# Kernel tuning notes

Measured on AMD Instinct MI355X. Metric: run time of the kernel, lower is better.

The kernel has to match this reference:

```python
import jax, jax.numpy as jnp
import numpy as np


def _layernorm(x, g, b, eps=1e-5):
    mu = jnp.mean(x, axis=-1, keepdims=True)
    xc = x - mu
    var = jnp.mean(xc * xc, axis=-1, keepdims=True)
    return xc * jax.lax.rsqrt(var + eps) * g + b


def _s5(u, Lambda_re, Lambda_im, B_re, B_im, C_re, C_im, Dskip, log_step):
    # Diagonal complex SSM with ZOH discretization (S5).
    Lam = Lambda_re + 1j * Lambda_im                       # (P,) complex64
    Lam_bar = jnp.exp(Lam * jnp.exp(log_step))             # (P,)
    B_bar = ((Lam_bar - 1.0) / Lam)[:, None] * (B_re + 1j * B_im)  # (P, D)
    Bu = jnp.einsum('bld,pd->blp', u.astype(jnp.complex64), B_bar)  # (B, L, P)
    A = jnp.broadcast_to(Lam_bar, Bu.shape)

    def combine(e1, e2):
        a1, b1 = e1
        a2, b2 = e2
        return a1 * a2, a2 * b1 + b2

    _, xs = jax.lax.associative_scan(combine, (A, Bu), axis=1)  # parallel scan over L
    y = 2.0 * jnp.real(jnp.einsum('blp,dp->bld', xs, C_re + 1j * C_im))
    return y + Dskip * u


def setup_inputs() -> dict:
    key = jax.random.key(0)
    ks = jax.random.split(key, 10)
    B, L, D, P = 4, 2048, 1024, 64
    F = int(D * 2.0)  # ff_mult = 2.0
    x = jax.random.normal(ks[0], (B, L, D), jnp.float32)
    ln1_g = jnp.ones((D,), jnp.float32)
    ln1_b = jnp.zeros((D,), jnp.float32)
    ln2_g = jnp.ones((D,), jnp.float32)
    ln2_b = jnp.zeros((D,), jnp.float32)
    Lambda_re = -(0.5 + jax.random.uniform(ks[1], (P,), jnp.float32))  # stable poles
    Lambda_im = jnp.pi * jnp.arange(P, dtype=jnp.float32)              # HiPPO-like spread
    B_re = jax.random.normal(ks[2], (P, D), jnp.float32) / np.float32(np.sqrt(D))
    B_im = jax.random.normal(ks[3], (P, D), jnp.float32) / np.float32(np.sqrt(D))
    C_re = jax.random.normal(ks[4], (D, P), jnp.float32) / np.float32(np.sqrt(P))
    C_im = jax.random.normal(ks[5], (D, P), jnp.float32) / np.float32(np.sqrt(P))
    Dskip = jax.random.normal(ks[6], (D,), jnp.float32)
    dt_min, dt_max = 1e-3, 1e-1
    log_step = (np.float32(np.log(dt_min))
                + jax.random.uniform(ks[7], (P,), jnp.float32)
                * np.float32(np.log(dt_max) - np.log(dt_min)))
    W_enc = jax.random.normal(ks[8], (2 * F, D), jnp.float32) / np.float32(np.sqrt(D))
    W_dec = jax.random.normal(ks[9], (D, F), jnp.float32) / np.float32(np.sqrt(F))
    return dict(x=x, ln1_g=ln1_g, ln1_b=ln1_b, ln2_g=ln2_g, ln2_b=ln2_b,
                Lambda_re=Lambda_re, Lambda_im=Lambda_im, B_re=B_re, B_im=B_im,
                C_re=C_re, C_im=C_im, Dskip=Dskip, log_step=log_step,
                W_enc=W_enc, W_dec=W_dec)


def reference(x, ln1_g, ln1_b, ln2_g, ln2_b, Lambda_re, Lambda_im, B_re, B_im,
              C_re, C_im, Dskip, log_step, W_enc, W_dec):
    # S5Block: pre-LN -> S5 -> GELU -> residual (dropout = identity in eval)
    fx = _layernorm(x, ln1_g, ln1_b)
    h = jax.nn.gelu(_s5(fx, Lambda_re, Lambda_im, B_re, B_im, C_re, C_im, Dskip, log_step),
                    approximate=False) + fx
    # pre-LN GEGLU feed-forward -> residual
    fx2 = _layernorm(h, ln2_g, ln2_b)
    e = fx2 @ W_enc.T                      # (B, L, 2F)
    a, gate = jnp.split(e, 2, axis=-1)
    e = a * jax.nn.gelu(gate, approximate=False)
    return e @ W_dec.T + fx2
```

## Files before the change

### kernel.cpp

```cpp
#include <hip/hip_runtime.h>
#include <hip/hip_bf16.h>
#include <math.h>

typedef unsigned short u16;
typedef __bf16 v8bf __attribute__((ext_vector_type(8)));
typedef float f32x4 __attribute__((ext_vector_type(4)));

__device__ __forceinline__ float us2f(u16 h) {
    union { unsigned int u; float f; } v; v.u = ((unsigned int)h) << 16; return v.f;
}
__device__ __forceinline__ u16 f2us(float f) {
    union { float f; unsigned int u; } v; v.f = f;
    unsigned int r = v.u + 0x7fffu + ((v.u >> 16) & 1u);
    return (u16)(r >> 16);
}
__device__ __forceinline__ float gelu_f(float x) {
    return 0.5f * x * (1.0f + erff(x * 0.70710678118654752f));
}
__device__ __forceinline__ void gload_lds16(const u16* g, u16* l) {
    auto gp = reinterpret_cast<const __attribute__((address_space(1))) unsigned int*>(
        (uintptr_t)g);
    auto lp = reinterpret_cast<__attribute__((address_space(3))) unsigned int*>(
        (uintptr_t)l);
    __builtin_amdgcn_global_load_lds(gp, lp, 16, 0, 0);
}

__global__ __launch_bounds__(256) void cvt_kernel(const float* __restrict__ in,
                                                  u16* __restrict__ out, int n)
{
    const int i = (blockIdx.x * 256 + threadIdx.x) * 8;
    if (i >= n) return;
    float4 a = *reinterpret_cast<const float4*>(in + i);
    float4 b = *reinterpret_cast<const float4*>(in + i + 4);
    u16 o[8] = { f2us(a.x), f2us(a.y), f2us(a.z), f2us(a.w),
                 f2us(b.x), f2us(b.y), f2us(b.z), f2us(b.w) };
    *reinterpret_cast<uint4*>(out + i) = *reinterpret_cast<uint4*>(o);
}

template<typename TIN>
__global__ __launch_bounds__(256) void ln_kernel(const TIN* __restrict__ in,
                                                 const float* __restrict__ g,
                                                 const float* __restrict__ b,
                                                 u16* __restrict__ out)
{
    const int row = blockIdx.x, tid = threadIdx.x;
    const size_t base = (size_t)row * 1024 + tid * 4;
    float x0, x1, x2, x3;
    if constexpr (sizeof(TIN) == 4) {
        float4 v = *reinterpret_cast<const float4*>(in + base);
        x0 = v.x; x1 = v.y; x2 = v.z; x3 = v.w;
    } else {
        ushort4 v = *reinterpret_cast<const ushort4*>((const u16*)in + base);
        x0 = us2f(v.x); x1 = us2f(v.y); x2 = us2f(v.z); x3 = us2f(v.w);
    }
    float s = x0 + x1 + x2 + x3;
    float q = x0*x0 + x1*x1 + x2*x2 + x3*x3;
    #pragma unroll
    for (int o = 32; o; o >>= 1) { s += __shfl_down(s, o); q += __shfl_down(q, o); }
    __shared__ float red[8];
    if ((tid & 63) == 0) { red[tid >> 6] = s; red[4 + (tid >> 6)] = q; }
    __syncthreads();
    s = red[0] + red[1] + red[2] + red[3];
    q = red[4] + red[5] + red[6] + red[7];
    const float mu = s * (1.0f / 1024.0f);
    const float rs = rsqrtf(q * (1.0f / 1024.0f) - mu * mu + 1e-5f);
    float4 gv = *reinterpret_cast<const float4*>(g + tid * 4);
    float4 bv = *reinterpret_cast<const float4*>(b + tid * 4);
    ushort4 o4;
    o4.x = f2us((x0 - mu) * rs * gv.x + bv.x);
    o4.y = f2us((x1 - mu) * rs * gv.y + bv.y);
    o4.z = f2us((x2 - mu) * rs * gv.z + bv.z);
    o4.w = f2us((x3 - mu) * rs * gv.w + bv.w);
    *reinterpret_cast<ushort4*>(out + base) = o4;
}

__global__ __launch_bounds__(256) void prep_kernel(
    const float* __restrict__ Lre, const float* __restrict__ Lim, const float* __restrict__ lstep,
    const float* __restrict__ Bre, const float* __restrict__ Bim,
    const float* __restrict__ Cre, const float* __restrict__ Cim,
    u16* __restrict__ Bbar, u16* __restrict__ C2)
{
    const int idx = blockIdx.x * 256 + threadIdx.x;
    if (idx < 65536) {
        const int p = idx >> 10, d = idx & 1023;
        const float lr = Lre[p], li = Lim[p];
        const float dt = expf(lstep[p]);
        const float er = expf(lr * dt);
        const float ar = er * cosf(li * dt), ai = er * sinf(li * dt);
        const float nr = ar - 1.0f, ni = ai;
        const float den = lr * lr + li * li;
        const float cr = (nr * lr + ni * li) / den;
        const float ci = (ni * lr - nr * li) / den;
        const float br = Bre[idx], bi = Bim[idx];
        Bbar[p * 1024 + d]        = f2us(cr * br - ci * bi);
        Bbar[(64 + p) * 1024 + d] = f2us(cr * bi + ci * br);
    } else {
        const int i = idx - 65536;
        const int d = i >> 6, p = i & 63;
        C2[d * 128 + p]      = f2us( 2.0f * Cre[i]);
        C2[d * 128 + 64 + p] = f2us(-2.0f * Cim[i]);
    }
}

__global__ __launch_bounds__(256) void scan_kernel(
    const float* __restrict__ Bu,
    const float* __restrict__ Lre, const float* __restrict__ Lim, const float* __restrict__ lstep,
    u16* __restrict__ A2)
{
    const int b = blockIdx.x >> 6;
    const int p = blockIdx.x & 63;
    const int t = threadIdx.x;
    const float lr = Lre[p], li = Lim[p];
    const float dt = expf(lstep[p]);
    const float er = expf(lr * dt);
    const float ar = er * cosf(li * dt), ai = er * sinf(li * dt);

    const size_t base = ((size_t)b * 2048 + t * 8) * 128;
    float xr[8], xi[8];
    float sr = 0.f, si = 0.f;
    #pragma unroll
    for (int i = 0; i < 8; ++i) {
        const float br = Bu[base + i * 128 + p];
        const float bi = Bu[base + i * 128 + 64 + p];
        const float nr = ar * sr - ai * si + br;
        const float ni = ar * si + ai * sr + bi;
        sr = nr; si = ni;
        xr[i] = sr; xi[i] = si;
    }
    float fr = ar, fi = ai;
    #pragma unroll
    for (int s = 0; s < 3; ++s) { const float t2 = fr*fr - fi*fi; fi = 2.f*fr*fi; fr = t2; }
    __shared__ float Er[256], Ei[256];
    Er[t] = sr; Ei[t] = si;
    __syncthreads();
    float vr = sr, vi = si;
    for (int off = 1; off < 256; off <<= 1) {
        float pr = 0.f, pi = 0.f;
        if (t >= off) { pr = Er[t - off]; pi = Ei[t - off]; }
        __syncthreads();
        vr += fr * pr - fi * pi;
        vi += fr * pi + fi * pr;
        Er[t] = vr; Ei[t] = vi;
        const float nf = fr*fr - fi*fi; fi = 2.f*fr*fi; fr = nf;
        __syncthreads();
    }
    float cr = 0.f, ci = 0.f;
    if (t > 0) { cr = Er[t - 1]; ci = Ei[t - 1]; }
    float gr = ar * cr - ai * ci, gi = ar * ci + ai * cr;
    #pragma unroll
    for (int i = 0; i < 8; ++i) {
        xr[i] += gr; xi[i] += gi;
        const float n2 = ar * gr - ai * gi; gi = ar * gi + ai * gr; gr = n2;
    }
    #pragma unroll
    for (int i = 0; i < 8; ++i) {
        const size_t m = (size_t)b * 2048 + t * 8 + i;
        A2[m * 128 + p]      = f2us(xr[i]);
        A2[m * 128 + 64 + p] = f2us(xi[i]);
    }
}

template<int BM, int BN>
__global__ __launch_bounds__(64) void gemm_small_kernel(
    const u16* __restrict__ A, const u16* __restrict__ B, float* __restrict__ Cout,
    const int N, const int K)
{
    __shared__ u16 lsA[BM * 32];
    __shared__ u16 lsB[BN * 32];
    const int tid = threadIdx.x;
    const int lane = tid & 63;
    const int m0 = blockIdx.y * BM, n0 = blockIdx.x * BN;
    f32x4 acc[4][4] = {};
    for (int k0 = 0; k0 < K; k0 += 32) {
        #pragma unroll
        for (int j = 0; j < 4; ++j) {
            const int s = j * 64 + tid;
            gload_lds16(A + (size_t)(m0 + (s >> 2)) * K + k0 + (s & 3) * 8,
                        lsA + (s - lane) * 8);
            gload_lds16(B + (size_t)(n0 + (s >> 2)) * K + k0 + (s & 3) * 8,
                        lsB + (s - lane) * 8);
        }
        __syncthreads();
        v8bf af[4], bfv[4];
        #pragma unroll
        for (int f = 0; f < 4; ++f)
            af[f] = *reinterpret_cast<const v8bf*>(
                lsA + (f * 16 + (lane & 15)) * 32 + (lane >> 4) * 8);
        #pragma unroll
        for (int f = 0; f < 4; ++f)
            bfv[f] = *reinterpret_cast<const v8bf*>(
                lsB + (f * 16 + (lane & 15)) * 32 + (lane >> 4) * 8);
        #pragma unroll
        for (int fm = 0; fm < 4; ++fm)
            #pragma unroll
            for (int fn = 0; fn < 4; ++fn)
                acc[fm][fn] = __builtin_amdgcn_mfma_f32_16x16x32_bf16(
                    af[fm], bfv[fn], acc[fm][fn], 0, 0, 0);
        __syncthreads();
    }
    #pragma unroll
    for (int fm = 0; fm < 4; ++fm)
    #pragma unroll
    for (int fn = 0; fn < 4; ++fn)
    #pragma unroll
    for (int i = 0; i < 4; ++i) {
        const int r = m0 + fm * 16 + (lane >> 4) * 4 + i;
        const int c = n0 + fn * 16 + (lane & 15);
        Cout[(size_t)r * N + c] = acc[fm][fn][i];
    }
}

template<bool GLU>
__device__ __forceinline__ void stage_half(u16* ldsbuf,
    const u16* __restrict__ A, const u16* __restrict__ Bm,
    int half, int tile, int m0, int n0, int K, int NO, int wid, int lane)
{
    const int k0 = tile * 64;
    #pragma unroll
    for (int j = 0; j < 2; ++j) {
        const int chunk = wid * 2 + j;
        const int rloc  = chunk * 8 + (lane >> 3);
        const int sslot = (lane & 7) ^ ((lane >> 3) & 7);
        const u16* src;
        int ldsrow0;
        if (half < 2) {
            ldsrow0 = half * 128 + chunk * 8;
            src = A + (size_t)(m0 + half * 128 + rloc) * K + k0 + sslot * 8;
        } else {
            const int rb = (half - 2) * 128 + rloc;
            ldsrow0 = 256 + (half - 2) * 128 + chunk * 8;
            const int grow = GLU ? ((half == 2) ? (n0 + rb) : (NO + n0 + rb - 128))
                                 : (n0 + rb);
            src = Bm + (size_t)grow * K + k0 + sslot * 8;
        }
        gload_lds16(src, ldsbuf + ldsrow0 * 64);
    }
}

template<int BROWS, int EPI, int NBX>
__global__ __launch_bounds__(512, 2) void gemm8p_kernel(
    const u16* __restrict__ A, const u16* __restrict__ Bm, void* __restrict__ Cout,
    const int K, const int NO, const int NT,
    const u16* __restrict__ aux, const float* __restrict__ dskip)
{
    constexpr bool GLU = (EPI == 2);
    __shared__ u16 lds[2][(256 + BROWS) * 64];

    const int tid  = threadIdx.x;
    const int lane = tid & 63;
    const int wid  = tid >> 6;
    const int wm   = wid >> 2;
    const int wn   = wid & 3;
    const int l15 = lane & 15, lg = lane >> 4, l7 = lane & 7;

    const int bid = blockIdx.x;
    const int swz = (bid & 7) * (NBX * 4) + (bid >> 3);
    const int by = swz / NBX, bx = swz % NBX;
    const int m0 = by * 256, n0 = bx * 128;

    f32x4 accA[8][2] = {};
    f32x4 accG[8][2] = {};

    constexpr int S_HALF[8] = {0, 1, 2, 3, 0, 1, 2, 3};
    constexpr int S_OFS [8] = {1, 1, 2, 2, 2, 2, 3, 3};

    #pragma unroll
    for (int t = 0; t < 2; ++t)
        #pragma unroll
        for (int h = 0; h < (GLU ? 4 : 3); ++h)
            stage_half<GLU>((u16*)lds[t], A, Bm, h, t, m0, n0, K, NO, wid, lane);
    asm volatile("s_waitcnt vmcnt(0)" ::: "memory");
    __builtin_amdgcn_s_barrier();

    const int NI = NT >> 1;
    for (int i = 0; i < NI; ++i) {
        #pragma unroll
        for (int hb = 0; hb < 2; ++hb) {
            const u16* cb = (const u16*)lds[hb];
            v8bf bf[2][2][2];
            #pragma unroll
            for (int p = 0; p < 4; ++p) {
                v8bf af[2][2];
                #pragma unroll
                for (int j = 0; j < 2; ++j) {
                    const int row = wm * 128 + (p * 2 + j) * 16 + l15;
                    #pragma unroll
                    for (int kk = 0; kk < 2; ++kk) {
                        const int phys = (kk * 4 + lg) ^ l7;
                        af[j][kk] = *reinterpret_cast<const v8bf*>(
                            cb + row * 64 + phys * 8);
                    }
                }
                if (p == 0) {
                    #pragma unroll
                    for (int cf = 0; cf < 2; ++cf)
                    #pragma unroll
                    for (int ag = 0; ag < (GLU ? 2 : 1); ++ag)
                    #pragma unroll
                    for (int kk = 0; kk < 2; ++kk) {
                        const int rb = ag * 128 + wn * 32 + cf * 16 + l15;
                        const int phys = (kk * 4 + lg) ^ l7;
                        bf[cf][ag][kk] = *reinterpret_cast<const v8bf*>(
                            cb + (256 + rb) * 64 + phys * 8);
                    }
                }
                {
                    const int ph = hb * 4 + p;
                    const int ofs = S_OFS[ph], sh = S_HALF[ph];
                    const int tgt = 2 * i + ofs;
                    bool dost = (ofs == 1) ? (i > 0) : (tgt < NT);
                    if (!GLU && sh == 3) dost = false;
                    if (dost)
                        stage_half<GLU>((u16*)lds[tgt & 1], A, Bm, sh, tgt,
                                        m0, n0, K, NO, wid, lane);
                }
                __builtin_amdgcn_s_barrier();
                asm volatile("s_waitcnt lgkmcnt(0)" ::: "memory");
                __builtin_amdgcn_sched_barrier(0);
                __builtin_amdgcn_s_setprio(1);
                #pragma unroll
                for (int j = 0; j < 2; ++j) {
                    const int mf = p * 2 + j;
                    #pragma unroll
                    for (int cf = 0; cf < 2; ++cf)
                    #pragma unroll
                    for (int kk = 0; kk < 2; ++kk) {
                        accA[mf][cf] = __builtin_amdgcn_mfma_f32_16x16x32_bf16(
                            af[j][kk], bf[cf][0][kk], accA[mf][cf], 0, 0, 0);
                        if constexpr (GLU)
                            accG[mf][cf] = __builtin_amdgcn_mfma_f32_16x16x32_bf16(
                                af[j][kk], bf[cf][1][kk], accG[mf][cf], 0, 0, 0);
                    }
                }
                __builtin_amdgcn_s_setprio(0);
                if (p == 3) {
                    const int keept = 2 * i + 2 + hb;
                    if (keept < NT) {
                        if constexpr (GLU)
                            asm volatile("s_waitcnt vmcnt(4)" ::: "memory");
                        else
                            asm volatile("s_waitcnt vmcnt(2)" ::: "memory");
                    } else {
                        asm volatile("s_waitcnt vmcnt(0)" ::: "memory");
                    }
                }
                __builtin_amdgcn_s_barrier();
            }
        }
    }

    #pragma unroll
    for (int mf = 0; mf < 8; ++mf)
    #pragma unroll
    for (int cf = 0; cf < 2; ++cf)
    #pragma unroll
    for (int q = 0; q < 4; ++q) {
        const int r = m0 + wm * 128 + mf * 16 + lg * 4 + q;
        const int c = n0 + wn * 32 + cf * 16 + l15;
        const size_t o = (size_t)r * NO + c;
        const float v = accA[mf][cf][q];
        if constexpr (EPI == 2) {
            ((u16*)Cout)[o] = f2us(v * gelu_f(accG[mf][cf][q]));
        } else if constexpr (EPI == 1) {
            const float u = us2f(aux[o]);
            const float t2 = v + dskip[c] * u;
            ((u16*)Cout)[o] = f2us(gelu_f(t2) + u);
        } else {
            ((float*)Cout)[o] = v + us2f(aux[o]);
        }
    }
}

static constexpr size_t OFF_FX  = 0;
static constexpr size_t OFF_BU  = 16777216;
static constexpr size_t OFF_A2  = 20971520;
static constexpr size_t OFF_E2  = 0;
static constexpr size_t OFF_FX2 = 33554432;
static constexpr size_t OFF_BB  = 50331648;
static constexpr size_t OFF_C2  = 50593792;
static constexpr size_t OFF_WE  = 50855936;
static constexpr size_t OFF_WD  = 59244544;

extern "C" void kernel_launch(void* const* d_in, const int* in_sizes, int n_in,
                              void* d_out, int out_size, void* d_ws, size_t ws_size,
                              hipStream_t stream) {
    const float* x    = (const float*)d_in[0];
    const float* l1g  = (const float*)d_in[1];
    const float* l1b  = (const float*)d_in[2];
    const float* l2g  = (const float*)d_in[3];
    const float* l2b  = (const float*)d_in[4];
    const float* Lre  = (const float*)d_in[5];
    const float* Lim  = (const float*)d_in[6];
    const float* Bre  = (const float*)d_in[7];
    const float* Bim  = (const float*)d_in[8];
    const float* Cre  = (const float*)d_in[9];
    const float* Cim  = (const float*)d_in[10];
    const float* Dsk  = (const float*)d_in[11];
    const float* lst  = (const float*)d_in[12];
    const float* Wenc = (const float*)d_in[13];
    const float* Wdec = (const float*)d_in[14];
    float* out = (float*)d_out;

    char* ws = (char*)d_ws;
    u16*   fx   = (u16*)(ws + OFF_FX);
    float* Bu   = (float*)(ws + OFF_BU);
    u16*   A2   = (u16*)(ws + OFF_A2);
    u16*   e2   = (u16*)(ws + OFF_E2);
    u16*   fx2  = (u16*)(ws + OFF_FX2);
    u16*   Bbar = (u16*)(ws + OFF_BB);
    u16*   C2   = (u16*)(ws + OFF_C2);
    u16*   WeB  = (u16*)(ws + OFF_WE);
    u16*   WdB  = (u16*)(ws + OFF_WD);
    u16*   h    = (u16*)d_out;

    ln_kernel<float><<<8192, 256, 0, stream>>>(x, l1g, l1b, fx);
    cvt_kernel<<<2048, 256, 0, stream>>>(Wenc, WeB, 4096 * 1024);
    cvt_kernel<<<1024, 256, 0, stream>>>(Wdec, WdB, 1024 * 2048);
    prep_kernel<<<512, 256, 0, stream>>>(Lre, Lim, lst, Bre, Bim, Cre, Cim, Bbar, C2);
    gemm_small_kernel<64, 64><<<dim3(2, 128), 64, 0, stream>>>(
        fx, Bbar, Bu, 128, 1024);
    scan_kernel<<<256, 256, 0, stream>>>(Bu, Lre, Lim, lst, A2);
    gemm8p_kernel<128, 1, 8><<<256, 512, 0, stream>>>(
        A2, C2, h, 128, 1024, 2, fx, Dsk);
    ln_kernel<u16><<<8192, 256, 0, stream>>>(h, l2g, l2b, fx2);
    gemm8p_kernel<256, 2, 16><<<512, 512, 0, stream>>>(
        fx2, WeB, e2, 1024, 2048, 16, nullptr, nullptr);
    gemm8p_kernel<128, 3, 8><<<256, 512, 0, stream>>>(
        e2, WdB, out, 2048, 1024, 32, fx2, nullptr);

    (void)in_sizes; (void)n_in; (void)out_size; (void)ws_size;
}
```

Before: 220.8 us.

## Specialize GEMM kernels into GEGLU 8-phase and plain 4-phase pipelines, merge prep kernels

Splits the generic templated GEMM into two kernels. One is a GEGLU-specific kernel with an unrolled 8-phase schedule and precomputed, incrementing staging pointers. The other is a plain GEMM kernel with a 4-phase schedule that reads 4 A fragments per phase and uses a smaller LDS buffer. It also fuses the two weight-conversion launches and the SSM parameter prep into a single kernel to cut launch overhead. The intent is to reduce address arithmetic and barrier count in the hot loops. The coarser phases may expose more latency or raise register pressure.

```diff
diff --git a/kernel.cpp b/kernel.cpp
--- a/kernel.cpp
+++ b/kernel.cpp
@@ -25,62 +25,28 @@
     __builtin_amdgcn_global_load_lds(gp, lp, 16, 0, 0);
 }
 
-__global__ __launch_bounds__(256) void cvt_kernel(const float* __restrict__ in,
-                                                  u16* __restrict__ out, int n)
-{
-    const int i = (blockIdx.x * 256 + threadIdx.x) * 8;
-    if (i >= n) return;
-    float4 a = *reinterpret_cast<const float4*>(in + i);
-    float4 b = *reinterpret_cast<const float4*>(in + i + 4);
-    u16 o[8] = { f2us(a.x), f2us(a.y), f2us(a.z), f2us(a.w),
-                 f2us(b.x), f2us(b.y), f2us(b.z), f2us(b.w) };
-    *reinterpret_cast<uint4*>(out + i) = *reinterpret_cast<uint4*>(o);
-}
-
-template<typename TIN>
-__global__ __launch_bounds__(256) void ln_kernel(const TIN* __restrict__ in,
-                                                 const float* __restrict__ g,
-                                                 const float* __restrict__ b,
-                                                 u16* __restrict__ out)
-{
-    const int row = blockIdx.x, tid = threadIdx.x;
-    const size_t base = (size_t)row * 1024 + tid * 4;
-    float x0, x1, x2, x3;
-    if constexpr (sizeof(TIN) == 4) {
-        float4 v = *reinterpret_cast<const float4*>(in + base);
-        x0 = v.x; x1 = v.y; x2 = v.z; x3 = v.w;
-    } else {
-        ushort4 v = *reinterpret_cast<const ushort4*>((const u16*)in + base);
-        x0 = us2f(v.x); x1 = us2f(v.y); x2 = us2f(v.z); x3 = us2f(v.w);
-    }
-    float s = x0 + x1 + x2 + x3;
-    float q = x0*x0 + x1*x1 + x2*x2 + x3*x3;
-    #pragma unroll
-    for (int o = 32; o; o >>= 1) { s += __shfl_down(s, o); q += __shfl_down(q, o); }
-    __shared__ float red[8];
-    if ((tid & 63) == 0) { red[tid >> 6] = s; red[4 + (tid >> 6)] = q; }
-    __syncthreads();
-    s = red[0] + red[1] + red[2] + red[3];
-    q = red[4] + red[5] + red[6] + red[7];
-    const float mu = s * (1.0f / 1024.0f);
-    const float rs = rsqrtf(q * (1.0f / 1024.0f) - mu * mu + 1e-5f);
-    float4 gv = *reinterpret_cast<const float4*>(g + tid * 4);
-    float4 bv = *reinterpret_cast<const float4*>(b + tid * 4);
-    ushort4 o4;
-    o4.x = f2us((x0 - mu) * rs * gv.x + bv.x);
-    o4.y = f2us((x1 - mu) * rs * gv.y + bv.y);
-    o4.z = f2us((x2 - mu) * rs * gv.z + bv.z);
-    o4.w = f2us((x3 - mu) * rs * gv.w + bv.w);
-    *reinterpret_cast<ushort4*>(out + base) = o4;
-}
-
-__global__ __launch_bounds__(256) void prep_kernel(
-    const float* __restrict__ Lre, const float* __restrict__ Lim, const float* __restrict__ lstep,
+__global__ __launch_bounds__(256) void prepall_kernel(
+    const float* __restrict__ Wenc, u16* __restrict__ WeB,
+    const float* __restrict__ Wdec, u16* __restrict__ WdB,
+    const float* __restrict__ Lre, const float* __restrict__ Lim,
+    const float* __restrict__ lstep,
     const float* __restrict__ Bre, const float* __restrict__ Bim,
     const float* __restrict__ Cre, const float* __restrict__ Cim,
     u16* __restrict__ Bbar, u16* __restrict__ C2)
 {
-    const int idx = blockIdx.x * 256 + threadIdx.x;
+    const int b = blockIdx.x, tid = threadIdx.x;
+    if (b < 3072) {
+        const float* in = (b < 2048) ? Wenc : Wdec;
+        u16* outp = (b < 2048) ? WeB : WdB;
+        const int i = (b < 2048 ? b : b - 2048) * 2048 + tid * 8;
+        float4 a = *reinterpret_cast<const float4*>(in + i);
+        float4 c = *reinterpret_cast<const float4*>(in + i + 4);
+        u16 o[8] = { f2us(a.x), f2us(a.y), f2us(a.z), f2us(a.w),
+                     f2us(c.x), f2us(c.y), f2us(c.z), f2us(c.w) };
+        *reinterpret_cast<uint4*>(outp + i) = *reinterpret_cast<uint4*>(o);
+        return;
+    }
+    const int idx = (b - 3072) * 256 + tid;
     if (idx < 65536) {
         const int p = idx >> 10, d = idx & 1023;
         const float lr = Lre[p], li = Lim[p];
@@ -102,9 +68,47 @@
     }
 }
 
+template<typename TIN>
+__global__ __launch_bounds__(256) void ln_kernel(const TIN* __restrict__ in,
+                                                 const float* __restrict__ g,
+                                                 const float* __restrict__ b,
+                                                 u16* __restrict__ out)
+{
+    const int row = blockIdx.x, tid = threadIdx.x;
+    const size_t base = (size_t)row * 1024 + tid * 4;
+    float x0, x1, x2, x3;
+    if constexpr (sizeof(TIN) == 4) {
+        float4 v = *reinterpret_cast<const float4*>(in + base);
+        x0 = v.x; x1 = v.y; x2 = v.z; x3 = v.w;
+    } else {
+        ushort4 v = *reinterpret_cast<const ushort4*>((const u16*)in + base);
+        x0 = us2f(v.x); x1 = us2f(v.y); x2 = us2f(v.z); x3 = us2f(v.w);
+    }
+    float s = x0 + x1 + x2 + x3;
+    float q = x0*x0 + x1*x1 + x2*x2 + x3*x3;
+    #pragma unroll
+    for (int o = 32; o; o >>= 1) { s += __shfl_down(s, o); q += __shfl_down(q, o); }
+    __shared__ float red[8];
+    if ((tid & 63) == 0) { red[tid >> 6] = s; red[4 + (tid >> 6)] = q; }
+    __syncthreads();
+    s = red[0] + red[1] + red[2] + red[3];
+    q = red[4] + red[5] + red[6] + red[7];
+    const float mu = s * (1.0f / 1024.0f);
+    const float rs = rsqrtf(q * (1.0f / 1024.0f) - mu * mu + 1e-5f);
+    float4 gv = *reinterpret_cast<const float4*>(g + tid * 4);
+    float4 bv = *reinterpret_cast<const float4*>(b + tid * 4);
+    ushort4 o4;
+    o4.x = f2us((x0 - mu) * rs * gv.x + bv.x);
+    o4.y = f2us((x1 - mu) * rs * gv.y + bv.y);
+    o4.z = f2us((x2 - mu) * rs * gv.z + bv.z);
+    o4.w = f2us((x3 - mu) * rs * gv.w + bv.w);
+    *reinterpret_cast<ushort4*>(out + base) = o4;
+}
+
 __global__ __launch_bounds__(256) void scan_kernel(
     const float* __restrict__ Bu,
-    const float* __restrict__ Lre, const float* __restrict__ Lim, const float* __restrict__ lstep,
+    const float* __restrict__ Lre, const float* __restrict__ Lim,
+    const float* __restrict__ lstep,
     u16* __restrict__ A2)
 {
     const int b = blockIdx.x >> 6;
@@ -210,143 +214,254 @@
     }
 }
 
-template<bool GLU>
-__device__ __forceinline__ void stage_half(u16* ldsbuf,
-    const u16* __restrict__ A, const u16* __restrict__ Bm,
-    int half, int tile, int m0, int n0, int K, int NO, int wid, int lane)
-{
-    const int k0 = tile * 64;
+#define BAR_MMA_BEGIN \
+    __builtin_amdgcn_s_barrier(); \
+    asm volatile("s_waitcnt lgkmcnt(0)" ::: "memory"); \
+    __builtin_amdgcn_sched_barrier(0); \
+    __builtin_amdgcn_s_setprio(1);
+#define MMA_END  __builtin_amdgcn_s_setprio(0);
+#define ENDBAR   __builtin_amdgcn_s_barrier();
+#define VMK(n)   asm volatile("s_waitcnt vmcnt(" #n ")" ::: "memory");
+
+#define STAGE(s, bi) do { \
+    u16* d0_ = lds + (bi) * BUFE + ((s) * 128 + (wid * 2 + 0) * 8) * 64; \
+    u16* d1_ = lds + (bi) * BUFE + ((s) * 128 + (wid * 2 + 1) * 8) * 64; \
+    gload_lds16(pS[s][0], d0_); gload_lds16(pS[s][1], d1_); \
+    pS[s][0] += 64; pS[s][1] += 64; } while (0)
+
+template<int MFB>
+__device__ __forceinline__ void glu_read_a(const u16* cb, int wm, int l15, int lg,
+                                           int l7, v8bf (&af)[2][2])
+{
     #pragma unroll
     for (int j = 0; j < 2; ++j) {
-        const int chunk = wid * 2 + j;
-        const int rloc  = chunk * 8 + (lane >> 3);
-        const int sslot = (lane & 7) ^ ((lane >> 3) & 7);
-        const u16* src;
-        int ldsrow0;
-        if (half < 2) {
-            ldsrow0 = half * 128 + chunk * 8;
-            src = A + (size_t)(m0 + half * 128 + rloc) * K + k0 + sslot * 8;
-        } else {
-            const int rb = (half - 2) * 128 + rloc;
-            ldsrow0 = 256 + (half - 2) * 128 + chunk * 8;
-            const int grow = GLU ? ((half == 2) ? (n0 + rb) : (NO + n0 + rb - 128))
-                                 : (n0 + rb);
-            src = Bm + (size_t)grow * K + k0 + sslot * 8;
-        }
-        gload_lds16(src, ldsbuf + ldsrow0 * 64);
-    }
-}
-
-template<int BROWS, int EPI, int NBX>
-__global__ __launch_bounds__(512, 2) void gemm8p_kernel(
-    const u16* __restrict__ A, const u16* __restrict__ Bm, void* __restrict__ Cout,
-    const int K, const int NO, const int NT,
-    const u16* __restrict__ aux, const float* __restrict__ dskip)
-{
-    constexpr bool GLU = (EPI == 2);
-    __shared__ u16 lds[2][(256 + BROWS) * 64];
-
-    const int tid  = threadIdx.x;
-    const int lane = tid & 63;
-    const int wid  = tid >> 6;
-    const int wm   = wid >> 2;
-    const int wn   = wid & 3;
+        const int row = wm * 128 + (MFB + j) * 16 + l15;
+        #pragma unroll
+        for (int kk = 0; kk < 2; ++kk)
+            af[j][kk] = *reinterpret_cast<const v8bf*>(
+                cb + row * 64 + (((kk * 4 + lg) ^ l7) * 8));
+    }
+}
+__device__ __forceinline__ void glu_read_b(const u16* cb, int wn, int l15, int lg,
+                                           int l7, v8bf (&bf)[2][2][2])
+{
+    #pragma unroll
+    for (int cf = 0; cf < 2; ++cf)
+    #pragma unroll
+    for (int ag = 0; ag < 2; ++ag)
+    #pragma unroll
+    for (int kk = 0; kk < 2; ++kk) {
+        const int rb = ag * 128 + wn * 32 + cf * 16 + l15;
+        bf[cf][ag][kk] = *reinterpret_cast<const v8bf*>(
+            cb + (256 + rb) * 64 + (((kk * 4 + lg) ^ l7) * 8));
+    }
+}
+template<int MFB>
+__device__ __forceinline__ void glu_mma(const v8bf (&af)[2][2], const v8bf (&bf)[2][2][2],
+                                        f32x4 (&accA)[8][2], f32x4 (&accG)[8][2])
+{
+    #pragma unroll
+    for (int j = 0; j < 2; ++j)
+    #pragma unroll
+    for (int cf = 0; cf < 2; ++cf)
+    #pragma unroll
+    for (int kk = 0; kk < 2; ++kk) {
+        accA[MFB + j][cf] = __builtin_amdgcn_mfma_f32_16x16x32_bf16(
+            af[j][kk], bf[cf][0][kk], accA[MFB + j][cf], 0, 0, 0);
+        accG[MFB + j][cf] = __builtin_amdgcn_mfma_f32_16x16x32_bf16(
+            af[j][kk], bf[cf][1][kk], accG[MFB + j][cf], 0, 0, 0);
+    }
+}
+
+template<int NBX>
+__global__ __launch_bounds__(512, 2) void geglu8p_kernel(
+    const u16* __restrict__ A, const u16* __restrict__ Bm, u16* __restrict__ Cout,
+    const int K, const int NO, const int NT)
+{
+    constexpr int BUFE = 512 * 64;
+    __shared__ u16 lds[2 * BUFE];
+    const int tid = threadIdx.x, lane = tid & 63, wid = tid >> 6;
+    const int wm = wid >> 2, wn = wid & 3;
     const int l15 = lane & 15, lg = lane >> 4, l7 = lane & 7;
-
     const int bid = blockIdx.x;
     const int swz = (bid & 7) * (NBX * 4) + (bid >> 3);
     const int by = swz / NBX, bx = swz % NBX;
     const int m0 = by * 256, n0 = bx * 128;
 
+    const int rl = lane >> 3;
+    const int scol = ((lane & 7) ^ rl) * 8;
+    const u16* pS[4][2];
+    #pragma unroll
+    for (int j = 0; j < 2; ++j) {
+        const int rloc = (wid * 2 + j) * 8 + rl;
+        pS[0][j] = A  + (size_t)(m0 + rloc)       * K + scol;
+        pS[1][j] = A  + (size_t)(m0 + 128 + rloc) * K + scol;
+        pS[2][j] = Bm + (size_t)(n0 + rloc)       * K + scol;
+        pS[3][j] = Bm + (size_t)(NO + n0 + rloc)  * K + scol;
+    }
+
     f32x4 accA[8][2] = {};
     f32x4 accG[8][2] = {};
 
-    constexpr int S_HALF[8] = {0, 1, 2, 3, 0, 1, 2, 3};
-    constexpr int S_OFS [8] = {1, 1, 2, 2, 2, 2, 3, 3};
-
-    #pragma unroll
-    for (int t = 0; t < 2; ++t)
-        #pragma unroll
-        for (int h = 0; h < (GLU ? 4 : 3); ++h)
-            stage_half<GLU>((u16*)lds[t], A, Bm, h, t, m0, n0, K, NO, wid, lane);
-    asm volatile("s_waitcnt vmcnt(0)" ::: "memory");
+    #pragma unroll
+    for (int t = 0; t < 2; ++t) {
+        STAGE(0, t); STAGE(1, t); STAGE(2, t); STAGE(3, t);
+    }
+    VMK(0);
     __builtin_amdgcn_s_barrier();
 
     const int NI = NT >> 1;
     for (int i = 0; i < NI; ++i) {
-        #pragma unroll
-        for (int hb = 0; hb < 2; ++hb) {
-            const u16* cb = (const u16*)lds[hb];
+        const bool s1 = (i > 0);
+        const bool s2 = (2 * i + 2 < NT);
+        const bool s3 = (2 * i + 3 < NT);
+        {
+            const u16* cb = lds;
             v8bf bf[2][2][2];
-            #pragma unroll
-            for (int p = 0; p < 4; ++p) {
-                v8bf af[2][2];
-                #pragma unroll
-                for (int j = 0; j < 2; ++j) {
-                    const int row = wm * 128 + (p * 2 + j) * 16 + l15;
-                    #pragma unroll
-                    for (int kk = 0; kk < 2; ++kk) {
-                        const int phys = (kk * 4 + lg) ^ l7;
-                        af[j][kk] = *reinterpret_cast<const v8bf*>(
-                            cb + row * 64 + phys * 8);
-                    }
-                }
-                if (p == 0) {
-                    #pragma unroll
-                    for (int cf = 0; cf < 2; ++cf)
-                    #pragma unroll
-                    for (int ag = 0; ag < (GLU ? 2 : 1); ++ag)
-                    #pragma unroll
-                    for (int kk = 0; kk < 2; ++kk) {
-                        const int rb = ag * 128 + wn * 32 + cf * 16 + l15;
-                        const int phys = (kk * 4 + lg) ^ l7;
-                        bf[cf][ag][kk] = *reinterpret_cast<const v8bf*>(
-                            cb + (256 + rb) * 64 + phys * 8);
-                    }
-                }
-                {
-                    const int ph = hb * 4 + p;
-                    const int ofs = S_OFS[ph], sh = S_HALF[ph];
-                    const int tgt = 2 * i + ofs;
-                    bool dost = (ofs == 1) ? (i > 0) : (tgt < NT);
-                    if (!GLU && sh == 3) dost = false;
-                    if (dost)
-                        stage_half<GLU>((u16*)lds[tgt & 1], A, Bm, sh, tgt,
-                                        m0, n0, K, NO, wid, lane);
-                }
-                __builtin_amdgcn_s_barrier();
-                asm volatile("s_waitcnt lgkmcnt(0)" ::: "memory");
-                __builtin_amdgcn_sched_barrier(0);
-                __builtin_amdgcn_s_setprio(1);
-                #pragma unroll
-                for (int j = 0; j < 2; ++j) {
-                    const int mf = p * 2 + j;
-                    #pragma unroll
-                    for (int cf = 0; cf < 2; ++cf)
-                    #pragma unroll
-                    for (int kk = 0; kk < 2; ++kk) {
-                        accA[mf][cf] = __builtin_amdgcn_mfma_f32_16x16x32_bf16(
-                            af[j][kk], bf[cf][0][kk], accA[mf][cf], 0, 0, 0);
-                        if constexpr (GLU)
-                            accG[mf][cf] = __builtin_amdgcn_mfma_f32_16x16x32_bf16(
-                                af[j][kk], bf[cf][1][kk], accG[mf][cf], 0, 0, 0);
-                    }
-                }
-                __builtin_amdgcn_s_setprio(0);
-                if (p == 3) {
-                    const int keept = 2 * i + 2 + hb;
-                    if (keept < NT) {
-                        if constexpr (GLU)
-                            asm volatile("s_waitcnt vmcnt(4)" ::: "memory");
-                        else
-                            asm volatile("s_waitcnt vmcnt(2)" ::: "memory");
-                    } else {
-                        asm volatile("s_waitcnt vmcnt(0)" ::: "memory");
-                    }
-                }
-                __builtin_amdgcn_s_barrier();
-            }
+            v8bf af[2][2];
+            glu_read_a<0>(cb, wm, l15, lg, l7, af);
+            glu_read_b(cb, wn, l15, lg, l7, bf);
+            if (s1) STAGE(0, 1);
+            BAR_MMA_BEGIN; glu_mma<0>(af, bf, accA, accG); MMA_END; ENDBAR;
+            glu_read_a<2>(cb, wm, l15, lg, l7, af);
+            if (s1) STAGE(1, 1);
+            BAR_MMA_BEGIN; glu_mma<2>(af, bf, accA, accG); MMA_END; ENDBAR;
+            glu_read_a<4>(cb, wm, l15, lg, l7, af);
+            if (s2) STAGE(2, 0);
+            BAR_MMA_BEGIN; glu_mma<4>(af, bf, accA, accG); MMA_END; ENDBAR;
+            glu_read_a<6>(cb, wm, l15, lg, l7, af);
+            if (s2) STAGE(3, 0);
+            BAR_MMA_BEGIN; glu_mma<6>(af, bf, accA, accG); MMA_END;
+            if (s2) { VMK(4); } else { VMK(0); }
+            ENDBAR;
         }
+        {
+            const u16* cb = lds + BUFE;
+            v8bf bf[2][2][2];
+            v8bf af[2][2];
+            glu_read_a<0>(cb, wm, l15, lg, l7, af);
+            glu_read_b(cb, wn, l15, lg, l7, bf);
+            if (s2) STAGE(0, 0);
+            BAR_MMA_BEGIN; glu_mma<0>(af, bf, accA, accG); MMA_END; ENDBAR;
+            glu_read_a<2>(cb, wm, l15, lg, l7, af);
+            if (s2) STAGE(1, 0);
+            BAR_MMA_BEGIN; glu_mma<2>(af, bf, accA, accG); MMA_END; ENDBAR;
+            glu_read_a<4>(cb, wm, l15, lg, l7, af);
+            if (s3) STAGE(2, 1);
+            BAR_MMA_BEGIN; glu_mma<4>(af, bf, accA, accG); MMA_END; ENDBAR;
+            glu_read_a<6>(cb, wm, l15, lg, l7, af);
+            if (s3) STAGE(3, 1);
+            BAR_MMA_BEGIN; glu_mma<6>(af, bf, accA, accG); MMA_END;
+            if (s3) { VMK(4); } else { VMK(0); }
+            ENDBAR;
+        }
+    }
+
+    #pragma unroll
+    for (int mf = 0; mf < 8; ++mf)
+    #pragma unroll
+    for (int cf = 0; cf < 2; ++cf)
+    #pragma unroll
+    for (int q = 0; q < 4; ++q) {
+        const int r = m0 + wm * 128 + mf * 16 + lg * 4 + q;
+        const int c = n0 + wn * 32 + cf * 16 + l15;
+        Cout[(size_t)r * NO + c] = f2us(accA[mf][cf][q] * gelu_f(accG[mf][cf][q]));
+    }
+}
+
+template<int MFB, bool READB>
+__device__ __forceinline__ void p4_read(const u16* cb, int wm, int wn, int l15,
+                                        int lg, int l7, v8bf (&af)[4][2], v8bf (&bf)[2][2])
+{
+    #pragma unroll
+    for (int j = 0; j < 4; ++j) {
+        const int row = wm * 128 + (MFB + j) * 16 + l15;
+        #pragma unroll
+        for (int kk = 0; kk < 2; ++kk)
+            af[j][kk] = *reinterpret_cast<const v8bf*>(
+                cb + row * 64 + (((kk * 4 + lg) ^ l7) * 8));
+    }
+    if constexpr (READB) {
+        #pragma unroll
+        for (int cf = 0; cf < 2; ++cf)
+        #pragma unroll
+        for (int kk = 0; kk < 2; ++kk) {
+            const int rb = wn * 32 + cf * 16 + l15;
+            bf[cf][kk] = *reinterpret_cast<const v8bf*>(
+                cb + (256 + rb) * 64 + (((kk * 4 + lg) ^ l7) * 8));
+        }
+    }
+}
+template<int MFB>
+__device__ __forceinline__ void p4_mma(const v8bf (&af)[4][2], const v8bf (&bf)[2][2],
+                                       f32x4 (&accA)[8][2])
+{
+    #pragma unroll
+    for (int j = 0; j < 4; ++j)
+    #pragma unroll
+    for (int cf = 0; cf < 2; ++cf)
+    #pragma unroll
+    for (int kk = 0; kk < 2; ++kk)
+        accA[MFB + j][cf] = __builtin_amdgcn_mfma_f32_16x16x32_bf16(
+            af[j][kk], bf[cf][kk], accA[MFB + j][cf], 0, 0, 0);
+}
+
+template<int EPI, int NBX>
+__global__ __launch_bounds__(512, 2) void gemm4p_kernel(
+    const u16* __restrict__ A, const u16* __restrict__ Bm, void* __restrict__ Cout,
+    const int K, const int NO, const int NT,
+    const u16* __restrict__ aux, const float* __restrict__ dskip)
+{
+    constexpr int BUFE = 384 * 64;
+    __shared__ u16 lds[2 * BUFE];
+    const int tid = threadIdx.x, lane = tid & 63, wid = tid >> 6;
+    const int wm = wid >> 2, wn = wid & 3;
+    const int l15 = lane & 15, lg = lane >> 4, l7 = lane & 7;
+    const int bid = blockIdx.x;
+    const int swz = (bid & 7) * (NBX * 4) + (bid >> 3);
+    const int by = swz / NBX, bx = swz % NBX;
+    const int m0 = by * 256, n0 = bx * 128;
+
+    const int rl = lane >> 3;
+    const int scol = ((lane & 7) ^ rl) * 8;
+    const u16* pS[3][2];
+    #pragma unroll
+    for (int j = 0; j < 2; ++j) {
+        const int rloc = (wid * 2 + j) * 8 + rl;
+        pS[0][j] = A  + (size_t)(m0 + rloc)       * K + scol;
+        pS[1][j] = A  + (size_t)(m0 + 128 + rloc) * K + scol;
+        pS[2][j] = Bm + (size_t)(n0 + rloc)       * K + scol;
+    }
+
+    f32x4 accA[8][2] = {};
+
+    #pragma unroll
+    for (int t = 0; t < 2; ++t) { STAGE(0, t); STAGE(1, t); STAGE(2, t); }
+    VMK(0);
+    __builtin_amdgcn_s_barrier();
+
+    const int NI = NT >> 1;
+    for (int i = 0; i < NI; ++i) {
+        const bool s1 = (i > 0);
+        const bool s2 = (2 * i + 2 < NT);
+        const bool s3 = (2 * i + 3 < NT);
+        v8bf af[4][2], bf[2][2];
+        p4_read<0, true>(lds, wm, wn, l15, lg, l7, af, bf);
+        if (s1) { STAGE(0, 1); STAGE(1, 1); }
+        BAR_MMA_BEGIN; p4_mma<0>(af, bf, accA); MMA_END; ENDBAR;
+        p4_read<4, false>(lds, wm, wn, l15, lg, l7, af, bf);
+        if (s2) STAGE(2, 0);
+        BAR_MMA_BEGIN; p4_mma<4>(af, bf, accA); MMA_END;
+        if (s2) { VMK(2); } else { VMK(0); }
+        ENDBAR;
+        p4_read<0, true>(lds + BUFE, wm, wn, l15, lg, l7, af, bf);
+        if (s2) { STAGE(0, 0); STAGE(1, 0); }
+        BAR_MMA_BEGIN; p4_mma<0>(af, bf, accA); MMA_END; ENDBAR;
+        p4_read<4, false>(lds + BUFE, wm, wn, l15, lg, l7, af, bf);
+        if (s3) STAGE(2, 1);
+        BAR_MMA_BEGIN; p4_mma<4>(af, bf, accA); MMA_END;
+        if (s3) { VMK(2); } else { VMK(0); }
+        ENDBAR;
     }
 
     #pragma unroll
@@ -359,9 +474,7 @@
         const int c = n0 + wn * 32 + cf * 16 + l15;
         const size_t o = (size_t)r * NO + c;
         const float v = accA[mf][cf][q];
-        if constexpr (EPI == 2) {
-            ((u16*)Cout)[o] = f2us(v * gelu_f(accG[mf][cf][q]));
-        } else if constexpr (EPI == 1) {
+        if constexpr (EPI == 1) {
             const float u = us2f(aux[o]);
             const float t2 = v + dskip[c] * u;
             ((u16*)Cout)[o] = f2us(gelu_f(t2) + u);
@@ -414,18 +527,17 @@
     u16*   h    = (u16*)d_out;
 
     ln_kernel<float><<<8192, 256, 0, stream>>>(x, l1g, l1b, fx);
-    cvt_kernel<<<2048, 256, 0, stream>>>(Wenc, WeB, 4096 * 1024);
-    cvt_kernel<<<1024, 256, 0, stream>>>(Wdec, WdB, 1024 * 2048);
-    prep_kernel<<<512, 256, 0, stream>>>(Lre, Lim, lst, Bre, Bim, Cre, Cim, Bbar, C2);
+    prepall_kernel<<<3584, 256, 0, stream>>>(Wenc, WeB, Wdec, WdB,
+                                             Lre, Lim, lst, Bre, Bim, Cre, Cim,
+                                             Bbar, C2);
     gemm_small_kernel<64, 64><<<dim3(2, 128), 64, 0, stream>>>(
         fx, Bbar, Bu, 128, 1024);
     scan_kernel<<<256, 256, 0, stream>>>(Bu, Lre, Lim, lst, A2);
-    gemm8p_kernel<128, 1, 8><<<256, 512, 0, stream>>>(
+    gemm4p_kernel<1, 8><<<256, 512, 0, stream>>>(
         A2, C2, h, 128, 1024, 2, fx, Dsk);
     ln_kernel<u16><<<8192, 256, 0, stream>>>(h, l2g, l2b, fx2);
-    gemm8p_kernel<256, 2, 16><<<512, 512, 0, stream>>>(
-        fx2, WeB, e2, 1024, 2048, 16, nullptr, nullptr);
-    gemm8p_kernel<128, 3, 8><<<256, 512, 0, stream>>>(
+    geglu8p_kernel<16><<<512, 512, 0, stream>>>(fx2, WeB, e2, 1024, 2048, 16);
+    gemm4p_kernel<3, 8><<<256, 512, 0, stream>>>(
         e2, WdB, out, 2048, 1024, 32, fx2, nullptr);
 
     (void)in_sizes; (void)n_in; (void)out_size; (void)ws_size;
```

Result: no change. 219.2 us (-0.7%).
